# Kernel tuning notes

Hardware: AMD Instinct MI355X
Metric: run time of the kernel (lower is better)

Reference implementation:

```python
import jax, jax.numpy as jnp
import numpy as np

NUM_JOINTS = 32
N_E = 1024
E_DIM = 128
BETA = 0.25
HID = 256
CHAINS = [[0,1,2,3,4,5],[0,6,7,8,9,10],[0,11,12,13,14,15],
          [12,16,17,18,19,20,21,22,23],[12,24,25,26,27,28,29,30,31]]


def setup_inputs() -> dict:
    key = jax.random.key(0)
    ks = jax.random.split(key, 8)
    B, T = 64, 128
    z = jax.random.normal(ks[0], (B, T, NUM_JOINTS, E_DIM), jnp.float32)
    # xavier_uniform for embeddings: bound = sqrt(6/(n_e+e_dim))
    eb = float(np.sqrt(6.0 / (N_E + E_DIM)))
    emb = jax.random.uniform(ks[1], (NUM_JOINTS, N_E, E_DIM), jnp.float32, -eb, eb)
    # torch Linear default init: U(-1/sqrt(fan_in), 1/sqrt(fan_in))
    b1b = float(1.0 / np.sqrt(2 * E_DIM))
    W1 = jax.random.uniform(ks[2], (2 * E_DIM, HID), jnp.float32, -b1b, b1b)
    b1 = jax.random.uniform(ks[3], (HID,), jnp.float32, -b1b, b1b)
    ln_g = jnp.ones((HID,), jnp.float32)
    ln_b = jnp.zeros((HID,), jnp.float32)
    b2b = float(1.0 / np.sqrt(HID))
    W2 = jax.random.uniform(ks[4], (HID, E_DIM), jnp.float32, -b2b, b2b)
    b2 = jax.random.uniform(ks[5], (E_DIM,), jnp.float32, -b2b, b2b)
    return {"z": z, "emb": emb, "W1": W1, "b1": b1, "ln_g": ln_g,
            "ln_b": ln_b, "W2": W2, "b2": b2}


def _layernorm(x, g, b, eps=1e-5):
    m = jnp.mean(x, axis=-1, keepdims=True)
    v = jnp.mean((x - m) ** 2, axis=-1, keepdims=True)
    return (x - m) * jax.lax.rsqrt(v + eps) * g + b


def _mlp(x, W1, b1, ln_g, ln_b, W2, b2):
    h = x @ W1 + b1
    h = jax.nn.relu(_layernorm(h, ln_g, ln_b))
    return h @ W2 + b2


def _quantize_joint(h, E):
    # h: [B,T,C], E: [n_e,C]. argmin of euclidean dist == argmin of -2 h.E^T + |E|^2
    B, T, C = h.shape
    hf = h.reshape(-1, C)
    d = -2.0 * (hf @ E.T) + jnp.sum(E * E, axis=1)  # [B*T, n_e]
    idx = jnp.argmin(d, axis=1)
    e = E[idx].reshape(B, T, C)  # one-hot @ E == gather
    sg = jax.lax.stop_gradient
    loss = jnp.mean((sg(e) - h) ** 2) + BETA * jnp.mean((e - sg(h)) ** 2)
    q = h + sg(e - h)  # straight-through
    return q, e, idx.reshape(B, T), loss


def reference(z, emb, W1, b1, ln_g, ln_b, W2, b2):
    B, T, V, C = z.shape
    sg = jax.lax.stop_gradient
    stored_q, stored_e, stored_idx = {}, {}, {}
    total = jnp.zeros((), z.dtype)
    for chain in CHAINS:
        parent_e = None
        for i, j in enumerate(chain):
            if j not in stored_q:  # single-pass per joint
                zj = z[:, :, j, :]
                h = _mlp(jnp.concatenate([parent_e, zj], -1), W1, b1, ln_g, ln_b, W2, b2) if i > 0 else zj
                q, e, idx, loss = _quantize_joint(h, emb[j])
                stored_q[j], stored_e[j], stored_idx[j] = q, e, idx
                total = total + loss
            parent_e = sg(stored_e[j])
    z_q = jnp.stack([stored_q[v] for v in range(V)], axis=2)      # [B,T,V,C]
    indices = jnp.stack([stored_idx[v] for v in range(V)], axis=2)  # [B,T,V]
    return z_q, total / V, indices
```

## Files before the change

kernel.cpp:

```cpp
#include <hip/hip_runtime.h>

#define NJ 32
#define NE 1024
#define CD 128
#define HID 256
#define ROWS 8192

struct Lv { int nj; int j[5]; int p[5]; };

__global__ __launch_bounds__(256) void norms_kernel(const float* __restrict__ emb,
                                                    float* __restrict__ nrm) {
  int gid = blockIdx.x * 256 + threadIdx.x;
  int n = gid >> 2, l = gid & 3;
  const float* row = emb + (size_t)n * CD;
  float s = 0.f;
#pragma unroll
  for (int i = 0; i < 8; ++i) {
    float4 v = *(const float4*)&row[(l + 4 * i) * 4];
    s += v.x * v.x + v.y * v.y + v.z * v.z + v.w * v.w;
  }
  s += __shfl_xor(s, 1);
  s += __shfl_xor(s, 2);
  if (l == 0) nrm[n] = s;
}

template <int RB>
__global__ __launch_bounds__(256, RB == 32 ? 4 : 3) void fused_level(
    const float* __restrict__ z, const float* __restrict__ emb,
    const float* __restrict__ W1, const float* __restrict__ b1,
    const float* __restrict__ lng, const float* __restrict__ lnb,
    const float* __restrict__ W2, const float* __restrict__ b2,
    const float* __restrict__ nrm,
    float* __restrict__ zq, float* __restrict__ idx_out,
    float* __restrict__ partials, Lv lv, int pbase) {
  constexpr int RPG = RB / 8;
  constexpr int HSP = RB + 4;
  constexpr int BPJ = ROWS / RB;
  constexpr int XS_SZ = 32 * HSP;
  constexpr int HS_SZ = 128 * HSP;
  constexpr int P1 = XS_SZ + 8448;
  constexpr int P3 = HS_SZ + 2112;
  constexpr int P4 = HS_SZ + 4128 + 512;
  constexpr int SM12 = (P1 > P3) ? P1 : P3;
  constexpr int SMEM = (SM12 > P4) ? SM12 : P4;

  __shared__ __align__(16) float smem[SMEM];
  __shared__ float wsum[4];
  float* xs  = smem;
  float* ws1 = smem + XS_SZ;
  float* as_ = smem;
  float* ws2 = smem + HS_SZ;
  float* hs  = smem;
  float* es  = smem + HS_SZ;
  float* nsm = smem + HS_SZ + 4128;

  const int tid = threadIdx.x;
  const int rg = tid >> 5, cg = tid & 31;
  const int u = cg & 15;
  const int qcA = (cg >> 4) * 128 + u * 4;
  const int qcB = qcA + 64;
  const int jl = blockIdx.x / BPJ;
  const int row0 = (blockIdx.x % BPJ) * RB;
  const int jj = lv.j[jl], pj = lv.p[jl];
  const size_t rstride = (size_t)NJ * CD;

  if (pj >= 0) {
    float acc1[RPG][8];
#pragma unroll
    for (int r = 0; r < RPG; ++r)
#pragma unroll
      for (int c = 0; c < 8; ++c) acc1[r][c] = 0.f;

#pragma unroll 1
    for (int ks = 0; ks < 8; ++ks) {
#pragma unroll
      for (int uu = 0; uu < RB / 32; ++uu) {
        int idx = uu * 256 + tid;
        int r = idx >> 3, kq = idx & 7;
        const float* src = (ks < 4)
            ? (zq + (size_t)(row0 + r) * rstride + (size_t)pj * CD + (ks * 32 + kq * 4))
            : (z  + (size_t)(row0 + r) * rstride + (size_t)jj * CD + (ks * 32 - 128 + kq * 4));
        float4 v = *(const float4*)src;
        xs[(kq * 4 + 0) * HSP + r] = v.x;
        xs[(kq * 4 + 1) * HSP + r] = v.y;
        xs[(kq * 4 + 2) * HSP + r] = v.z;
        xs[(kq * 4 + 3) * HSP + r] = v.w;
      }
#pragma unroll
      for (int v8 = 0; v8 < 8; ++v8) {
        int idx = v8 * 256 + tid;
        int k = idx >> 6, c4 = idx & 63;
        *(float4*)&ws1[k * 264 + c4 * 4] =
            *(const float4*)&W1[(size_t)(ks * 32 + k) * HID + c4 * 4];
      }
      __syncthreads();
#pragma unroll 2
      for (int kk = 0; kk < 32; ++kk) {
        float xr[RPG], wc[8];
#pragma unroll
        for (int g = 0; g < RPG / 4; ++g)
          *(float4*)&xr[g * 4] = *(const float4*)&xs[kk * HSP + rg * RPG + g * 4];
        *(float4*)&wc[0] = *(const float4*)&ws1[kk * 264 + qcA];
        *(float4*)&wc[4] = *(const float4*)&ws1[kk * 264 + qcB];
#pragma unroll
        for (int r = 0; r < RPG; ++r)
#pragma unroll
          for (int c = 0; c < 8; ++c)
            acc1[r][c] += xr[r] * wc[c];
      }
      __syncthreads();
    }

    {
      float bb[8], gg[8], be[8];
      *(float4*)&bb[0] = *(const float4*)&b1[qcA];
      *(float4*)&bb[4] = *(const float4*)&b1[qcB];
      *(float4*)&gg[0] = *(const float4*)&lng[qcA];
      *(float4*)&gg[4] = *(const float4*)&lng[qcB];
      *(float4*)&be[0] = *(const float4*)&lnb[qcA];
      *(float4*)&be[4] = *(const float4*)&lnb[qcB];
#pragma unroll
      for (int r = 0; r < RPG; ++r) {
        float s0 = 0.f, q0 = 0.f;
#pragma unroll
        for (int j = 0; j < 8; ++j) {
          float v = acc1[r][j] + bb[j];
          acc1[r][j] = v;
          s0 += v; q0 += v * v;
        }
        float si = __shfl_xor(s0, 16), qi = __shfl_xor(q0, 16);
        float s1 = si, q1 = qi;
#pragma unroll
        for (int j = 0; j < 8; ++j) {
          float v = acc1[r][j];
          s1 += v; q1 += v * v;
        }
#pragma unroll
        for (int m = 1; m < 16; m <<= 1) {
          s1 += __shfl_xor(s1, m); q1 += __shfl_xor(q1, m);
        }
        float s2 = __shfl_xor(s1, 16), q2 = __shfl_xor(q1, 16);
        float Sx = (cg & 16) ? s1 : s2;
        float Qx = (cg & 16) ? q1 : q2;
        float mu = Sx * (1.f / HID);
        float va = Qx * (1.f / HID) - mu * mu;
        float iv = 1.f / sqrtf(va + 1e-5f);
#pragma unroll
        for (int j = 0; j < 8; ++j) {
          float a = (acc1[r][j] - mu) * iv * gg[j] + be[j];
          acc1[r][j] = fmaxf(a, 0.f);
        }
      }
    }

    float acc2[RPG][4];
#pragma unroll
    for (int r = 0; r < RPG; ++r)
#pragma unroll
      for (int c = 0; c < 4; ++c) acc2[r][c] = 0.f;

#pragma unroll 1
    for (int half = 0; half < 2; ++half) {
      __syncthreads();
      if ((cg >> 4) == half) {
#pragma unroll
        for (int j = 0; j < 8; ++j) {
          int kl = (j >> 2) * 64 + u * 4 + (j & 3);
#pragma unroll
          for (int g = 0; g < RPG / 4; ++g)
            *(float4*)&as_[kl * HSP + rg * RPG + g * 4] =
                make_float4(acc1[g * 4 + 0][j], acc1[g * 4 + 1][j],
                            acc1[g * 4 + 2][j], acc1[g * 4 + 3][j]);
        }
      }
      __syncthreads();
#pragma unroll 1
      for (int kc = 0; kc < 8; ++kc) {
#pragma unroll
        for (int v = 0; v < 2; ++v) {
          int idx = v * 256 + tid;
          int k = idx >> 5, c4 = idx & 31;
          *(float4*)&ws2[k * 132 + c4 * 4] =
              *(const float4*)&W2[(size_t)(half * 128 + kc * 16 + k) * CD + c4 * 4];
        }
        __syncthreads();
#pragma unroll 2
        for (int kk = 0; kk < 16; ++kk) {
          float ar[RPG], wc2[4];
#pragma unroll
          for (int g = 0; g < RPG / 4; ++g)
            *(float4*)&ar[g * 4] =
                *(const float4*)&as_[(kc * 16 + kk) * HSP + rg * RPG + g * 4];
          *(float4*)&wc2[0] = *(const float4*)&ws2[kk * 132 + cg * 4];
#pragma unroll
          for (int r = 0; r < RPG; ++r)
#pragma unroll
            for (int c = 0; c < 4; ++c)
              acc2[r][c] += ar[r] * wc2[c];
        }
        __syncthreads();
      }
    }
    {
      float4 bv = *(const float4*)&b2[cg * 4];
      float bb2[4] = {bv.x, bv.y, bv.z, bv.w};
#pragma unroll
      for (int c = 0; c < 4; ++c) {
#pragma unroll
        for (int g = 0; g < RPG / 4; ++g)
          *(float4*)&hs[(cg * 4 + c) * HSP + rg * RPG + g * 4] =
              make_float4(acc2[g * 4 + 0][c] + bb2[c], acc2[g * 4 + 1][c] + bb2[c],
                          acc2[g * 4 + 2][c] + bb2[c], acc2[g * 4 + 3][c] + bb2[c]);
      }
    }
  } else {
#pragma unroll
    for (int v = 0; v < RB / 8; ++v) {
      int idx = v * 256 + tid;
      int r = idx >> 5, c4 = idx & 31;
      float4 vz = *(const float4*)&z[(size_t)(row0 + r) * rstride + (size_t)jj * CD + c4 * 4];
      hs[(c4 * 4 + 0) * HSP + r] = vz.x;
      hs[(c4 * 4 + 1) * HSP + r] = vz.y;
      hs[(c4 * 4 + 2) * HSP + r] = vz.z;
      hs[(c4 * 4 + 3) * HSP + r] = vz.w;
    }
  }

  float mnv[RPG]; int mni[RPG];
#pragma unroll
  for (int r = 0; r < RPG; ++r) { mnv[r] = 3.402823e38f; mni[r] = 0; }
  const float* embJ = emb + (size_t)jj * NE * CD;
  const float* nrmJ = nrm + jj * NE;

#pragma unroll 1
  for (int p = 0; p < 2; ++p) {
    __syncthreads();
    if (tid < 128) {
      *(float4*)&nsm[tid * 4] = *(const float4*)&nrmJ[p * 512 + tid * 4];
    }
    float acc4[RPG][16];
#pragma unroll
    for (int r = 0; r < RPG; ++r)
#pragma unroll
      for (int c = 0; c < 16; ++c) acc4[r][c] = 0.f;

#pragma unroll 1
    for (int kc = 0; kc < 16; ++kc) {
#pragma unroll
      for (int v = 0; v < 4; ++v) {
        int idx = v * 256 + tid;
        int n = idx >> 1, kq = idx & 1;
        float4 ev = *(const float4*)&embJ[(size_t)(p * 512 + n) * CD + kc * 8 + kq * 4];
        es[(kq * 4 + 0) * 516 + n] = ev.x;
        es[(kq * 4 + 1) * 516 + n] = ev.y;
        es[(kq * 4 + 2) * 516 + n] = ev.z;
        es[(kq * 4 + 3) * 516 + n] = ev.w;
      }
      __syncthreads();
#pragma unroll 2
      for (int kk = 0; kk < 8; ++kk) {
        int c = kc * 8 + kk;
        float hr[RPG], ec[16];
#pragma unroll
        for (int g = 0; g < RPG / 4; ++g)
          *(float4*)&hr[g * 4] = *(const float4*)&hs[c * HSP + rg * RPG + g * 4];
        *(float4*)&ec[0]  = *(const float4*)&es[kk * 516 + qcA];
        *(float4*)&ec[4]  = *(const float4*)&es[kk * 516 + qcB];
        *(float4*)&ec[8]  = *(const float4*)&es[kk * 516 + 256 + qcA];
        *(float4*)&ec[12] = *(const float4*)&es[kk * 516 + 256 + qcB];
#pragma unroll
        for (int r = 0; r < RPG; ++r)
#pragma unroll
          for (int c2 = 0; c2 < 16; ++c2)
            acc4[r][c2] += hr[r] * ec[c2];
      }
      __syncthreads();
    }
#pragma unroll
    for (int r = 0; r < RPG; ++r) {
#pragma unroll
      for (int q = 0; q < 4; ++q) {
        int o = ((q & 1) ? qcB : qcA) + (q >> 1) * 256;
#pragma unroll
        for (int cc = 0; cc < 4; ++cc) {
          int nl = o + cc;
          float d = nsm[nl] - 2.f * acc4[r][q * 4 + cc];
          int n = p * 512 + nl;
          if (d < mnv[r]) { mnv[r] = d; mni[r] = n; }
        }
      }
    }
  }

#pragma unroll
  for (int r = 0; r < RPG; ++r) {
    float mv = mnv[r]; int mi = mni[r];
#pragma unroll
    for (int m = 1; m < 32; m <<= 1) {
      float om = __shfl_xor(mv, m); int oi = __shfl_xor(mi, m);
      if (om < mv || (om == mv && oi < mi)) { mv = om; mi = oi; }
    }
    mnv[r] = mv; mni[r] = mi;
  }

  float lsum = 0.f;
#pragma unroll
  for (int r = 0; r < RPG; ++r) {
    int row = rg * RPG + r;
    int id = mni[r];
    const float* erow = embJ + (size_t)id * CD;
    float4 ev = *(const float4*)&erow[cg * 4];
    float h0 = hs[(cg * 4 + 0) * HSP + row];
    float h1 = hs[(cg * 4 + 1) * HSP + row];
    float h2 = hs[(cg * 4 + 2) * HSP + row];
    float h3 = hs[(cg * 4 + 3) * HSP + row];
    float dx = ev.x - h0, dy = ev.y - h1, dz = ev.z - h2, dw = ev.w - h3;
    lsum += dx * dx + dy * dy + dz * dz + dw * dw;
    *(float4*)&zq[(size_t)(row0 + row) * rstride + (size_t)jj * CD + cg * 4] = ev;
    if (cg == 0) idx_out[(size_t)(row0 + row) * NJ + jj] = (float)id;
  }
#pragma unroll
  for (int m = 1; m < 64; m <<= 1) lsum += __shfl_xor(lsum, m);
  if ((tid & 63) == 0) wsum[tid >> 6] = lsum;
  __syncthreads();
  if (tid == 0) partials[pbase + blockIdx.x] = wsum[0] + wsum[1] + wsum[2] + wsum[3];
}

__global__ __launch_bounds__(256) void loss_reduce(const float* __restrict__ p, int n,
                                                   float* __restrict__ out) {
  __shared__ float ws[4];
  float s = 0.f;
  for (int i = threadIdx.x; i < n; i += 256) s += p[i];
#pragma unroll
  for (int m = 1; m < 64; m <<= 1) s += __shfl_xor(s, m);
  if ((threadIdx.x & 63) == 0) ws[threadIdx.x >> 6] = s;
  __syncthreads();
  if (threadIdx.x == 0)
    out[0] = (ws[0] + ws[1] + ws[2] + ws[3]) * (1.25f / (1048576.f * 32.f));
}

extern "C" void kernel_launch(void* const* d_in, const int* in_sizes, int n_in,
                              void* d_out, int out_size, void* d_ws, size_t ws_size,
                              hipStream_t stream) {
  const float* z = (const float*)d_in[0];
  const float* emb = (const float*)d_in[1];
  const float* W1 = (const float*)d_in[2];
  const float* b1 = (const float*)d_in[3];
  const float* lng = (const float*)d_in[4];
  const float* lnb = (const float*)d_in[5];
  const float* W2 = (const float*)d_in[6];
  const float* b2 = (const float*)d_in[7];

  float* zq = (float*)d_out;
  float* loss = zq + (size_t)ROWS * NJ * CD;
  float* idxo = loss + 1;

  float* nrm = (float*)d_ws;
  float* partials = nrm + NJ * NE;

  norms_kernel<<<NJ * NE * 4 / 256, 256, 0, stream>>>(emb, nrm);

  static const Lv levels[11] = {
      {1, {0, 0, 0, 0, 0}, {-1, 0, 0, 0, 0}},
      {3, {1, 6, 11, 0, 0}, {0, 0, 0, 0, 0}},
      {3, {2, 7, 12, 0, 0}, {1, 6, 11, 0, 0}},
      {5, {3, 8, 13, 16, 24}, {2, 7, 12, 12, 12}},
      {5, {4, 9, 14, 17, 25}, {3, 8, 13, 16, 24}},
      {5, {5, 10, 15, 18, 26}, {4, 9, 14, 17, 25}},
      {2, {19, 27, 0, 0, 0}, {18, 26, 0, 0, 0}},
      {2, {20, 28, 0, 0, 0}, {19, 27, 0, 0, 0}},
      {2, {21, 29, 0, 0, 0}, {20, 28, 0, 0, 0}},
      {2, {22, 30, 0, 0, 0}, {21, 29, 0, 0, 0}},
      {2, {23, 31, 0, 0, 0}, {22, 30, 0, 0, 0}},
  };
  static const int rbs[11] = {32, 64, 64, 64, 64, 64, 32, 32, 32, 32, 32};

  int pbase = 0;
  for (int L = 0; L < 11; ++L) {
    int bpj = ROWS / rbs[L];
    int blocks = levels[L].nj * bpj;
    if (rbs[L] == 64) {
      fused_level<64><<<blocks, 256, 0, stream>>>(
          z, emb, W1, b1, lng, lnb, W2, b2, nrm, zq, idxo, partials, levels[L], pbase);
    } else {
      fused_level<32><<<blocks, 256, 0, stream>>>(
          z, emb, W1, b1, lng, lnb, W2, b2, nrm, zq, idxo, partials, levels[L], pbase);
    }
    pbase += blocks;
  }
  loss_reduce<<<1, 256, 0, stream>>>(partials, pbase, loss);
}
```

Baseline: 2.106 ms.

## Retile codebook distance GEMM to per-wave row blocks with wider k chunks

```diff
diff --git a/kernel.cpp b/kernel.cpp
--- a/kernel.cpp
+++ b/kernel.cpp
@@ -25,7 +25,7 @@
 }
 
 template <int RB>
-__global__ __launch_bounds__(256, RB == 32 ? 4 : 3) void fused_level(
+__global__ __launch_bounds__(256) void fused_level(
     const float* __restrict__ z, const float* __restrict__ emb,
     const float* __restrict__ W1, const float* __restrict__ b1,
     const float* __restrict__ lng, const float* __restrict__ lnb,
@@ -34,13 +34,14 @@
     float* __restrict__ zq, float* __restrict__ idx_out,
     float* __restrict__ partials, Lv lv, int pbase) {
   constexpr int RPG = RB / 8;
+  constexpr int R4 = RB / 4;
   constexpr int HSP = RB + 4;
   constexpr int BPJ = ROWS / RB;
   constexpr int XS_SZ = 32 * HSP;
   constexpr int HS_SZ = 128 * HSP;
   constexpr int P1 = XS_SZ + 8448;
   constexpr int P3 = HS_SZ + 2112;
-  constexpr int P4 = HS_SZ + 4128 + 512;
+  constexpr int P4 = HS_SZ + 16 * 516 + 512;
   constexpr int SM12 = (P1 > P3) ? P1 : P3;
   constexpr int SMEM = (SM12 > P4) ? SM12 : P4;
 
@@ -52,7 +53,7 @@
   float* ws2 = smem + HS_SZ;
   float* hs  = smem;
   float* es  = smem + HS_SZ;
-  float* nsm = smem + HS_SZ + 4128;
+  float* nsm = smem + HS_SZ + 16 * 516;
 
   const int tid = threadIdx.x;
   const int rg = tid >> 5, cg = tid & 31;
@@ -226,9 +227,11 @@
     }
   }
 
-  float mnv[RPG]; int mni[RPG];
-#pragma unroll
-  for (int r = 0; r < RPG; ++r) { mnv[r] = 3.402823e38f; mni[r] = 0; }
+  const int w4 = tid >> 6;
+  const int l4 = tid & 63;
+  float mnv[R4]; int mni[R4];
+#pragma unroll
+  for (int r = 0; r < R4; ++r) { mnv[r] = 3.402823e38f; mni[r] = 0; }
   const float* embJ = emb + (size_t)jj * NE * CD;
   const float* nrmJ = nrm + jj * NE;
 
@@ -238,19 +241,19 @@
     if (tid < 128) {
       *(float4*)&nsm[tid * 4] = *(const float4*)&nrmJ[p * 512 + tid * 4];
     }
-    float acc4[RPG][16];
-#pragma unroll
-    for (int r = 0; r < RPG; ++r)
-#pragma unroll
-      for (int c = 0; c < 16; ++c) acc4[r][c] = 0.f;
-
-#pragma unroll 1
-    for (int kc = 0; kc < 16; ++kc) {
-#pragma unroll
-      for (int v = 0; v < 4; ++v) {
+    float acc4[R4][8];
+#pragma unroll
+    for (int r = 0; r < R4; ++r)
+#pragma unroll
+      for (int c = 0; c < 8; ++c) acc4[r][c] = 0.f;
+
+#pragma unroll 1
+    for (int kc = 0; kc < 8; ++kc) {
+#pragma unroll
+      for (int v = 0; v < 8; ++v) {
         int idx = v * 256 + tid;
-        int n = idx >> 1, kq = idx & 1;
-        float4 ev = *(const float4*)&embJ[(size_t)(p * 512 + n) * CD + kc * 8 + kq * 4];
+        int n = idx >> 2, kq = idx & 3;
+        float4 ev = *(const float4*)&embJ[(size_t)(p * 512 + n) * CD + kc * 16 + kq * 4];
         es[(kq * 4 + 0) * 516 + n] = ev.x;
         es[(kq * 4 + 1) * 516 + n] = ev.y;
         es[(kq * 4 + 2) * 516 + n] = ev.z;
@@ -258,33 +261,30 @@
       }
       __syncthreads();
 #pragma unroll 2
-      for (int kk = 0; kk < 8; ++kk) {
-        int c = kc * 8 + kk;
-        float hr[RPG], ec[16];
-#pragma unroll
-        for (int g = 0; g < RPG / 4; ++g)
-          *(float4*)&hr[g * 4] = *(const float4*)&hs[c * HSP + rg * RPG + g * 4];
-        *(float4*)&ec[0]  = *(const float4*)&es[kk * 516 + qcA];
-        *(float4*)&ec[4]  = *(const float4*)&es[kk * 516 + qcB];
-        *(float4*)&ec[8]  = *(const float4*)&es[kk * 516 + 256 + qcA];
-        *(float4*)&ec[12] = *(const float4*)&es[kk * 516 + 256 + qcB];
-#pragma unroll
-        for (int r = 0; r < RPG; ++r)
-#pragma unroll
-          for (int c2 = 0; c2 < 16; ++c2)
+      for (int kk = 0; kk < 16; ++kk) {
+        int c = kc * 16 + kk;
+        float hr[R4], ec[8];
+#pragma unroll
+        for (int g = 0; g < R4 / 4; ++g)
+          *(float4*)&hr[g * 4] = *(const float4*)&hs[c * HSP + w4 * R4 + g * 4];
+        *(float4*)&ec[0] = *(const float4*)&es[kk * 516 + l4 * 4];
+        *(float4*)&ec[4] = *(const float4*)&es[kk * 516 + 256 + l4 * 4];
+#pragma unroll
+        for (int r = 0; r < R4; ++r)
+#pragma unroll
+          for (int c2 = 0; c2 < 8; ++c2)
             acc4[r][c2] += hr[r] * ec[c2];
       }
       __syncthreads();
     }
 #pragma unroll
-    for (int r = 0; r < RPG; ++r) {
-#pragma unroll
-      for (int q = 0; q < 4; ++q) {
-        int o = ((q & 1) ? qcB : qcA) + (q >> 1) * 256;
-#pragma unroll
-        for (int cc = 0; cc < 4; ++cc) {
-          int nl = o + cc;
-          float d = nsm[nl] - 2.f * acc4[r][q * 4 + cc];
+    for (int r = 0; r < R4; ++r) {
+#pragma unroll
+      for (int q = 0; q < 2; ++q) {
+#pragma unroll
+        for (int j = 0; j < 4; ++j) {
+          int nl = q * 256 + l4 * 4 + j;
+          float d = nsm[nl] - 2.f * acc4[r][q * 4 + j];
           int n = p * 512 + nl;
           if (d < mnv[r]) { mnv[r] = d; mni[r] = n; }
         }
@@ -293,10 +293,10 @@
   }
 
 #pragma unroll
-  for (int r = 0; r < RPG; ++r) {
+  for (int r = 0; r < R4; ++r) {
     float mv = mnv[r]; int mi = mni[r];
 #pragma unroll
-    for (int m = 1; m < 32; m <<= 1) {
+    for (int m = 1; m < 64; m <<= 1) {
       float om = __shfl_xor(mv, m); int oi = __shfl_xor(mi, m);
       if (om < mv || (om == mv && oi < mi)) { mv = om; mi = oi; }
     }
@@ -305,23 +305,21 @@
 
   float lsum = 0.f;
 #pragma unroll
-  for (int r = 0; r < RPG; ++r) {
-    int row = rg * RPG + r;
+  for (int r = 0; r < R4; ++r) {
+    int row = w4 * R4 + r;
     int id = mni[r];
     const float* erow = embJ + (size_t)id * CD;
-    float4 ev = *(const float4*)&erow[cg * 4];
-    float h0 = hs[(cg * 4 + 0) * HSP + row];
-    float h1 = hs[(cg * 4 + 1) * HSP + row];
-    float h2 = hs[(cg * 4 + 2) * HSP + row];
-    float h3 = hs[(cg * 4 + 3) * HSP + row];
-    float dx = ev.x - h0, dy = ev.y - h1, dz = ev.z - h2, dw = ev.w - h3;
-    lsum += dx * dx + dy * dy + dz * dz + dw * dw;
-    *(float4*)&zq[(size_t)(row0 + row) * rstride + (size_t)jj * CD + cg * 4] = ev;
-    if (cg == 0) idx_out[(size_t)(row0 + row) * NJ + jj] = (float)id;
+    float2 ev = *(const float2*)&erow[l4 * 2];
+    float h0 = hs[(l4 * 2 + 0) * HSP + row];
+    float h1 = hs[(l4 * 2 + 1) * HSP + row];
+    float dx = ev.x - h0, dy = ev.y - h1;
+    lsum += dx * dx + dy * dy;
+    *(float2*)&zq[(size_t)(row0 + row) * rstride + (size_t)jj * CD + l4 * 2] = ev;
+    if (l4 == r) idx_out[(size_t)(row0 + row) * NJ + jj] = (float)id;
   }
 #pragma unroll
   for (int m = 1; m < 64; m <<= 1) lsum += __shfl_xor(lsum, m);
-  if ((tid & 63) == 0) wsum[tid >> 6] = lsum;
+  if (l4 == 0) wsum[w4] = lsum;
   __syncthreads();
   if (tid == 0) partials[pbase + blockIdx.x] = wsum[0] + wsum[1] + wsum[2] + wsum[3];
 }
@@ -373,7 +371,7 @@
       {2, {22, 30, 0, 0, 0}, {21, 29, 0, 0, 0}},
       {2, {23, 31, 0, 0, 0}, {22, 30, 0, 0, 0}},
   };
-  static const int rbs[11] = {32, 64, 64, 64, 64, 64, 32, 32, 32, 32, 32};
+  static const int rbs[11] = {16, 64, 64, 64, 64, 64, 32, 32, 32, 32, 32};
 
   int pbase = 0;
   for (int L = 0; L < 11; ++L) {
@@ -382,9 +380,12 @@
     if (rbs[L] == 64) {
       fused_level<64><<<blocks, 256, 0, stream>>>(
           z, emb, W1, b1, lng, lnb, W2, b2, nrm, zq, idxo, partials, levels[L], pbase);
-    } else {
+    } else if (rbs[L] == 32) {
       fused_level<32><<<blocks, 256, 0, stream>>>(
           z, emb, W1, b1, lng, lnb, W2, b2, nrm, zq, idxo, partials, levels[L], pbase);
+    } else {
+      fused_level<16><<<blocks, 256, 0, stream>>>(
+          z, emb, W1, b1, lng, lnb, W2, b2, nrm, zq, idxo, partials, levels[L], pbase);
     }
     pbase += blocks;
   }
```

Result: faster. 1.877 ms (-10.9%).
